# Optimization experiments

Measured on AMD Instinct MI355X. Metric: run time of the kernel, lower is better.

The kernel has to match this reference:

```python
import jax, jax.numpy as jnp
import numpy as np

B, T, D, H, L = 16, 1500, 512, 1024, 20


def setup_inputs() -> dict:
    key = jax.random.key(0)
    ks = jax.random.split(key, 5)
    return {
        "x": jax.random.normal(ks[0], (B, T, D), dtype=jnp.float32),
        "w1": jax.random.normal(ks[1], (D, H), dtype=jnp.float32) * (1.0 / np.sqrt(D)),
        "b1": jax.random.normal(ks[2], (H,), dtype=jnp.float32) * 0.01,
        "wp": jax.random.normal(ks[3], (H, D), dtype=jnp.float32) * (1.0 / np.sqrt(H)),
        "wa": jax.random.normal(ks[4], (D, L), dtype=jnp.float32) * (1.0 / np.sqrt(D)),
    }


def reference(x, w1, b1, wp, wa):
    # x: [B,T,D]
    f1 = jax.nn.relu(x @ w1 + b1)          # [B,T,H]
    p1 = f1 @ wp                            # [B,T,D] (output_dim == input_dim)
    lorder = wa.shape[1]
    t = p1.shape[1]
    # left-pad time axis with lorder-1 zeros so shift i looks at p1[t-i]
    padded = jnp.pad(p1, ((0, 0), (lorder - 1, 0), (0, 0)))  # [B,T+L-1,D]
    # z[..., i] = p1 shifted back by i frames (zero for t-i < 0)
    z = jnp.stack(
        [jax.lax.dynamic_slice_in_dim(padded, lorder - 1 - i, t, axis=1)
         for i in range(lorder)],
        axis=-1,
    )  # [B,T,D,L]
    att = jax.nn.softmax(x @ wa, axis=-1)   # [B,T,L]
    out1 = jnp.einsum('btdl,btl->btd', z, att)
    return x + out1
```

## Files before the change

### kernel.cpp

```cpp
#include <hip/hip_runtime.h>
#include <hip/hip_bf16.h>

#define Bd 16
#define Td 1500
#define Dd 512
#define Hd 1024
#define Ld 20
#define Md (Bd*Td)

using f32x4  = __attribute__((ext_vector_type(4))) float;
using short8 = __attribute__((ext_vector_type(8))) short;

__device__ __forceinline__ unsigned short f2bf(float f) {
    union { float f; unsigned u; } v; v.f = f;
    unsigned r = v.u + 0x7fffu + ((v.u >> 16) & 1u);
    return (unsigned short)(r >> 16);
}
__device__ __forceinline__ float bf2f(unsigned short u) {
    union { unsigned u; float f; } v; v.u = ((unsigned)u) << 16;
    return v.f;
}
__device__ __forceinline__ void gload_lds16(const void* g, void* l) {
    __builtin_amdgcn_global_load_lds(
        (const __attribute__((address_space(1))) unsigned*)g,
        (__attribute__((address_space(3))) unsigned*)l, 16, 0, 0);
}

__global__ __launch_bounds__(256) void cvt_x_kernel(
    const float* __restrict__ in, unsigned short* __restrict__ out)
{
    size_t i = ((size_t)blockIdx.x * 256 + threadIdx.x) * 8;
    float4 v0 = *(const float4*)(in + i);
    float4 v1 = *(const float4*)(in + i + 4);
    union { unsigned short us[8]; int4 v; } p;
    p.us[0] = f2bf(v0.x); p.us[1] = f2bf(v0.y); p.us[2] = f2bf(v0.z); p.us[3] = f2bf(v0.w);
    p.us[4] = f2bf(v1.x); p.us[5] = f2bf(v1.y); p.us[6] = f2bf(v1.z); p.us[7] = f2bf(v1.w);
    *(int4*)(out + i) = p.v;
}

__global__ __launch_bounds__(256) void transpose_convert_k(
    const float* __restrict__ W, unsigned short* __restrict__ WT, int K, int N)
{
    __shared__ float tile[32][33];
    int n0 = blockIdx.x * 32, k0 = blockIdx.y * 32;
    int tx = threadIdx.x, ty = threadIdx.y;
#pragma unroll
    for (int j = 0; j < 32; j += 8)
        tile[ty + j][tx] = W[(size_t)(k0 + ty + j) * N + n0 + tx];
    __syncthreads();
#pragma unroll
    for (int j = 0; j < 32; j += 8)
        WT[(size_t)(n0 + ty + j) * K + k0 + tx] = f2bf(tile[tx][ty + j]);
}

__global__ __launch_bounds__(256) void prep_waT_kernel(
    const float* __restrict__ wa, unsigned short* __restrict__ waT)
{
    int i = blockIdx.x * 256 + threadIdx.x;
    int c = i >> 9, d = i & 511;
    waT[i] = (c < Ld) ? f2bf(wa[(size_t)d * Ld + c]) : (unsigned short)0;
}

template<bool RELU_BIAS>
__global__ __launch_bounds__(256) void gemm_lds(
    const unsigned short* __restrict__ A, const unsigned short* __restrict__ BT,
    const float* __restrict__ bias, unsigned short* __restrict__ C,
    int Mdim, int Ndim, int Kdim)
{
    __shared__ __align__(16) unsigned short SH[2][3][128 * 32];

    const int tid  = threadIdx.x;
    const int lane = tid & 63;
    const int wave = tid >> 6;
    const int wr   = wave >> 1, wc = wave & 1;

    const int nx  = gridDim.x;
    const int nwg = nx * gridDim.y;
    const int id  = blockIdx.y * nx + blockIdx.x;
    const int nid = (id & 7) * (nwg >> 3) + (id >> 3);
    const int m0  = (nid / nx) * 128;
    const int n0  = (nid % nx) * 128;

    const int srow  = tid >> 2;
    const int sslot = (tid & 3) ^ ((tid >> 3) & 3);
    int ar0 = m0 + srow;      if (ar0 >= Mdim) ar0 = Mdim - 1;
    int ar1 = m0 + 64 + srow; if (ar1 >= Mdim) ar1 = Mdim - 1;
    const unsigned short* a0p = A  + (size_t)ar0 * Kdim + sslot * 8;
    const unsigned short* a1p = A  + (size_t)ar1 * Kdim + sslot * 8;
    const unsigned short* b0p = BT + (size_t)(n0 + srow) * Kdim + sslot * 8;
    const unsigned short* b1p = BT + (size_t)(n0 + 64 + srow) * Kdim + sslot * 8;

    const int rsel = lane & 15;
    const int koff = ((lane >> 4) ^ ((lane >> 1) & 3)) * 8;

    f32x4 acc[4][4] = {};
    const int NT = Kdim >> 5;

    auto stage = [&](int t, int b) {
        const int kk = t * 32;
        gload_lds16(a0p + kk, &SH[0][b][wave * 512]);
        gload_lds16(a1p + kk, &SH[0][b][2048 + wave * 512]);
        gload_lds16(b0p + kk, &SH[1][b][wave * 512]);
        gload_lds16(b1p + kk, &SH[1][b][2048 + wave * 512]);
    };

    stage(0, 0);
    stage(1, 1);

    int buf = 0;
    for (int t = 0; t < NT; ++t) {
        if (t + 1 < NT) asm volatile("s_waitcnt vmcnt(4)" ::: "memory");
        else            asm volatile("s_waitcnt vmcnt(0)" ::: "memory");
        __builtin_amdgcn_s_barrier();
        asm volatile("" ::: "memory");

        if (t + 2 < NT) {
            int nb = buf + 2;
            if (nb >= 3) nb -= 3;
            stage(t + 2, nb);
        }

        const unsigned short* as = &SH[0][buf][0];
        const unsigned short* bs = &SH[1][buf][0];
        short8 af[4], bfr[4];
#pragma unroll
        for (int m = 0; m < 4; ++m)
            af[m] = *(const short8*)&as[(wr * 64 + m * 16 + rsel) * 32 + koff];
#pragma unroll
        for (int n = 0; n < 4; ++n)
            bfr[n] = *(const short8*)&bs[(wc * 64 + n * 16 + rsel) * 32 + koff];

        __builtin_amdgcn_s_setprio(1);
#pragma unroll
        for (int m = 0; m < 4; ++m)
#pragma unroll
            for (int n = 0; n < 4; ++n)
                acc[m][n] = __builtin_amdgcn_mfma_f32_16x16x32_bf16(af[m], bfr[n], acc[m][n], 0, 0, 0);
        __builtin_amdgcn_s_setprio(0);

        ++buf; if (buf == 3) buf = 0;
    }

    __syncthreads();
    unsigned short* Cs = (unsigned short*)SH;

    const int rB = wr * 64 + ((lane >> 4) << 2);
    const int cB = wc * 64;
#pragma unroll
    for (int n = 0; n < 4; ++n) {
        const int col = cB + n * 16 + rsel;
        float bvs = 0.f;
        if (RELU_BIAS) bvs = bias[n0 + col];
        const int s = col >> 3, e = col & 7;
#pragma unroll
        for (int m = 0; m < 4; ++m) {
#pragma unroll
            for (int j = 0; j < 4; ++j) {
                const int r = rB + m * 16 + j;
                float v = acc[m][n][j];
                if (RELU_BIAS) v = fmaxf(v + bvs, 0.f);
                Cs[r * 128 + ((s ^ (r & 7)) << 3) + e] = f2bf(v);
            }
        }
    }
    __syncthreads();

    const int row = tid >> 1;
    const int c0  = (tid & 1) * 64;
    const int gr  = m0 + row;
    if (gr < Mdim) {
#pragma unroll
        for (int i = 0; i < 8; ++i) {
            const int s = (c0 >> 3) + i;
            int4 v = *(const int4*)&Cs[row * 128 + ((s ^ (row & 7)) << 3)];
            *(int4*)&C[(size_t)gr * Ndim + n0 + c0 + i * 8] = v;
        }
    }
}

__global__ __launch_bounds__(256) void att_mfma_kernel(
    const unsigned short* __restrict__ xb, const unsigned short* __restrict__ waT,
    float* __restrict__ att)
{
    __shared__ __align__(16) unsigned short waTs[16 * 1024];
    __shared__ __align__(16) unsigned short As[3][64 * 32];
    __shared__ float sS[64][21];

    const int tid  = threadIdx.x;
    const int lane = tid & 63;
    const int wave = tid >> 6;
    const int m0   = blockIdx.x * 64;

    for (int i = tid; i < 2048; i += 256) {
        const int off = i * 8;
        const int kt = off >> 10, c = (off >> 5) & 31, sl = (off >> 3) & 3;
        const int ssl = sl ^ ((c >> 1) & 3);
        *(short8*)&waTs[off] = *(const short8*)&waT[(size_t)c * Dd + kt * 32 + ssl * 8];
    }
    __syncthreads();

    const int srow  = tid >> 2;
    const int sslot = (tid & 3) ^ ((tid >> 3) & 3);
    const unsigned short* a0p = xb + (size_t)(m0 + srow) * Dd + sslot * 8;

    const int rsel = lane & 15;
    const int koff = ((lane >> 4) ^ ((lane >> 1) & 3)) * 8;

    f32x4 acc[2] = {};

    gload_lds16(a0p, &As[0][wave * 512]);
    gload_lds16(a0p + 32, &As[1][wave * 512]);

    int buf = 0;
    for (int t = 0; t < 16; ++t) {
        if (t < 15) asm volatile("s_waitcnt vmcnt(1)" ::: "memory");
        else        asm volatile("s_waitcnt vmcnt(0)" ::: "memory");
        __builtin_amdgcn_s_barrier();
        asm volatile("" ::: "memory");

        if (t + 2 < 16) {
            int nb = buf + 2; if (nb >= 3) nb -= 3;
            gload_lds16(a0p + (t + 2) * 32, &As[nb][wave * 512]);
        }

        short8 af = *(const short8*)&As[buf][(wave * 16 + rsel) * 32 + koff];
        short8 b0 = *(const short8*)&waTs[t * 1024 + (rsel) * 32 + koff];
        short8 b1 = *(const short8*)&waTs[t * 1024 + (16 + rsel) * 32 + koff];
        acc[0] = __builtin_amdgcn_mfma_f32_16x16x32_bf16(af, b0, acc[0], 0, 0, 0);
        acc[1] = __builtin_amdgcn_mfma_f32_16x16x32_bf16(af, b1, acc[1], 0, 0, 0);

        ++buf; if (buf == 3) buf = 0;
    }

    const int r0 = wave * 16 + ((lane >> 4) << 2);
#pragma unroll
    for (int n = 0; n < 2; ++n) {
        const int c = n * 16 + rsel;
        if (c < 21) {
#pragma unroll
            for (int j = 0; j < 4; ++j)
                sS[r0 + j][c] = acc[n][j];
        }
    }
    __syncthreads();

    if (tid < 64) {
        float mx = -1e30f;
#pragma unroll
        for (int l = 0; l < Ld; ++l) mx = fmaxf(mx, sS[tid][l]);
        float e[Ld]; float sum = 0.f;
#pragma unroll
        for (int l = 0; l < Ld; ++l) { e[l] = __expf(sS[tid][l] - mx); sum += e[l]; }
        const float inv = 1.f / sum;
        const int grow = m0 + tid;
#pragma unroll
        for (int l = 0; l < Ld; ++l)
            att[(size_t)grow * Ld + l] = e[l] * inv;
    }
}

__global__ __launch_bounds__(512) void out_kernel(
    const float* __restrict__ x, const unsigned short* __restrict__ p1,
    const float* __restrict__ att, float* __restrict__ out)
{
    const int bid = blockIdx.x;
    const int nid = (bid & 7) * 375 + (bid >> 3);
    const int wave = threadIdx.x >> 6;
    const int lane = threadIdx.x & 63;
    const int row  = nid * 8 + wave;
    const int t    = row % Td;
    const int d0   = lane * 8;

    float av[Ld];
    const float* ar = att + (size_t)row * Ld;
#pragma unroll
    for (int i = 0; i < Ld; i += 4) {
        float4 v = *(const float4*)(ar + i);
        av[i] = v.x; av[i + 1] = v.y; av[i + 2] = v.z; av[i + 3] = v.w;
    }

    const float* xr = x + (size_t)row * Dd + d0;
    float4 xa = *(const float4*)xr;
    float4 xb4 = *(const float4*)(xr + 4);
    float acc[8] = { xa.x, xa.y, xa.z, xa.w, xb4.x, xb4.y, xb4.z, xb4.w };

    const int imax = (t < Ld - 1) ? t : (Ld - 1);
    const unsigned short* pr = p1 + (size_t)row * Dd + d0;
    for (int i = 0; i <= imax; ++i) {
        const float a = av[i];
        short8 p = *(const short8*)(pr - (size_t)i * Dd);
#pragma unroll
        for (int j = 0; j < 8; ++j) acc[j] += a * bf2f((unsigned short)p[j]);
    }
    float* orow = out + (size_t)row * Dd + d0;
    float4 o0 = { acc[0], acc[1], acc[2], acc[3] };
    float4 o1 = { acc[4], acc[5], acc[6], acc[7] };
    *(float4*)orow       = o0;
    *(float4*)(orow + 4) = o1;
}

extern "C" void kernel_launch(void* const* d_in, const int* in_sizes, int n_in,
                              void* d_out, int out_size, void* d_ws, size_t ws_size,
                              hipStream_t stream)
{
    const float* x  = (const float*)d_in[0];
    const float* w1 = (const float*)d_in[1];
    const float* b1 = (const float*)d_in[2];
    const float* wp = (const float*)d_in[3];
    const float* wa = (const float*)d_in[4];
    float* out = (float*)d_out;

    char* ws = (char*)d_ws;
    unsigned short* xb  = (unsigned short*)ws;  ws += (size_t)Md * Dd * 2;
    unsigned short* w1T = (unsigned short*)ws;  ws += (size_t)Hd * Dd * 2;
    unsigned short* wpT = (unsigned short*)ws;  ws += (size_t)Dd * Hd * 2;
    unsigned short* waT = (unsigned short*)ws;  ws += (size_t)32 * Dd * 2;
    unsigned short* f1  = (unsigned short*)ws;  ws += (size_t)Md * Hd * 2;
    unsigned short* p1  = (unsigned short*)ws;  ws += (size_t)Md * Dd * 2;
    float*          att = (float*)ws;           ws += (size_t)Md * Ld * 4;

    cvt_x_kernel<<<(Md * Dd) / 2048, 256, 0, stream>>>(x, xb);
    transpose_convert_k<<<dim3(Hd / 32, Dd / 32), dim3(32, 8), 0, stream>>>(w1, w1T, Dd, Hd);
    transpose_convert_k<<<dim3(Dd / 32, Hd / 32), dim3(32, 8), 0, stream>>>(wp, wpT, Hd, Dd);
    prep_waT_kernel<<<(32 * Dd) / 256, 256, 0, stream>>>(wa, waT);

    att_mfma_kernel<<<Md / 64, 256, 0, stream>>>(xb, waT, att);

    const int mtiles = (Md + 127) / 128;
    gemm_lds<true ><<<dim3(Hd / 128, mtiles), 256, 0, stream>>>(xb, w1T, b1, f1, Md, Hd, Dd);
    gemm_lds<false><<<dim3(Dd / 128, mtiles), 256, 0, stream>>>(f1, wpT, nullptr, p1, Md, Dd, Hd);

    out_kernel<<<Md / 8, 512, 0, stream>>>(x, p1, att, out);
}
```

Before: 226.5 us.

## Enlarge GEMM tiles to 256x128 with 512 threads and fuse prep kernels

The GEMM kernel moves from a 128x128 tile with 256 threads to a 256x128 tile with 512 threads (8 waves), so each B tile loaded into LDS is shared by twice as many rows. The goal is less global traffic per FLOP. The input conversion, the two weight transposes and the waT prep are merged into one launch, removing three kernel launches. In exchange the GEMM uses more LDS per block, has fewer blocks in flight, and has a larger partial tail tile at the M edge. The epilogue and wave-index code not shown must already handle 8 waves.

```diff
diff --git a/kernel.cpp b/kernel.cpp
--- a/kernel.cpp
+++ b/kernel.cpp
@@ -26,24 +26,11 @@
         (__attribute__((address_space(3))) unsigned*)l, 16, 0, 0);
 }
 
-__global__ __launch_bounds__(256) void cvt_x_kernel(
-    const float* __restrict__ in, unsigned short* __restrict__ out)
-{
-    size_t i = ((size_t)blockIdx.x * 256 + threadIdx.x) * 8;
-    float4 v0 = *(const float4*)(in + i);
-    float4 v1 = *(const float4*)(in + i + 4);
-    union { unsigned short us[8]; int4 v; } p;
-    p.us[0] = f2bf(v0.x); p.us[1] = f2bf(v0.y); p.us[2] = f2bf(v0.z); p.us[3] = f2bf(v0.w);
-    p.us[4] = f2bf(v1.x); p.us[5] = f2bf(v1.y); p.us[6] = f2bf(v1.z); p.us[7] = f2bf(v1.w);
-    *(int4*)(out + i) = p.v;
-}
-
-__global__ __launch_bounds__(256) void transpose_convert_k(
-    const float* __restrict__ W, unsigned short* __restrict__ WT, int K, int N)
-{
-    __shared__ float tile[32][33];
-    int n0 = blockIdx.x * 32, k0 = blockIdx.y * 32;
-    int tx = threadIdx.x, ty = threadIdx.y;
+__device__ __forceinline__ void transpose_body(
+    const float* __restrict__ W, unsigned short* __restrict__ WT,
+    int K, int N, int n0, int k0, int tid, float (*tile)[33])
+{
+    const int tx = tid & 31, ty = tid >> 5;
 #pragma unroll
     for (int j = 0; j < 32; j += 8)
         tile[ty + j][tx] = W[(size_t)(k0 + ty + j) * N + n0 + tx];
@@ -53,21 +40,42 @@
         WT[(size_t)(n0 + ty + j) * K + k0 + tx] = f2bf(tile[tx][ty + j]);
 }
 
-__global__ __launch_bounds__(256) void prep_waT_kernel(
-    const float* __restrict__ wa, unsigned short* __restrict__ waT)
-{
-    int i = blockIdx.x * 256 + threadIdx.x;
-    int c = i >> 9, d = i & 511;
-    waT[i] = (c < Ld) ? f2bf(wa[(size_t)d * Ld + c]) : (unsigned short)0;
+__global__ __launch_bounds__(256) void prep_kernel(
+    const float* __restrict__ x,  const float* __restrict__ w1,
+    const float* __restrict__ wp, const float* __restrict__ wa,
+    unsigned short* __restrict__ xb,  unsigned short* __restrict__ w1T,
+    unsigned short* __restrict__ wpT, unsigned short* __restrict__ waT)
+{
+    __shared__ float tile[32][33];
+    const int b = blockIdx.x, tid = threadIdx.x;
+    if (b < 6000) {
+        size_t i = ((size_t)b * 256 + tid) * 8;
+        float4 v0 = *(const float4*)(x + i);
+        float4 v1 = *(const float4*)(x + i + 4);
+        union { unsigned short us[8]; int4 v; } p;
+        p.us[0] = f2bf(v0.x); p.us[1] = f2bf(v0.y); p.us[2] = f2bf(v0.z); p.us[3] = f2bf(v0.w);
+        p.us[4] = f2bf(v1.x); p.us[5] = f2bf(v1.y); p.us[6] = f2bf(v1.z); p.us[7] = f2bf(v1.w);
+        *(int4*)(xb + i) = p.v;
+    } else if (b < 6512) {
+        const int idx = b - 6000;
+        transpose_body(w1, w1T, Dd, Hd, (idx & 31) * 32, (idx >> 5) * 32, tid, tile);
+    } else if (b < 7024) {
+        const int idx = b - 6512;
+        transpose_body(wp, wpT, Hd, Dd, (idx & 15) * 32, (idx >> 4) * 32, tid, tile);
+    } else {
+        const int i = (b - 7024) * 256 + tid;
+        const int c = i >> 9, d = i & 511;
+        waT[i] = (c < Ld) ? f2bf(wa[(size_t)d * Ld + c]) : (unsigned short)0;
+    }
 }
 
 template<bool RELU_BIAS>
-__global__ __launch_bounds__(256) void gemm_lds(
+__global__ __launch_bounds__(512) void gemm_lds(
     const unsigned short* __restrict__ A, const unsigned short* __restrict__ BT,
     const float* __restrict__ bias, unsigned short* __restrict__ C,
     int Mdim, int Ndim, int Kdim)
 {
-    __shared__ __align__(16) unsigned short SH[2][3][128 * 32];
+    __shared__ __align__(16) unsigned short SH[3 * 8192 + 3 * 4096];
 
     const int tid  = threadIdx.x;
     const int lane = tid & 63;
@@ -78,17 +86,16 @@
     const int nwg = nx * gridDim.y;
     const int id  = blockIdx.y * nx + blockIdx.x;
     const int nid = (id & 7) * (nwg >> 3) + (id >> 3);
-    const int m0  = (nid / nx) * 128;
+    const int m0  = (nid / nx) * 256;
     const int n0  = (nid % nx) * 128;
 
     const int srow  = tid >> 2;
-    const int sslot = (tid & 3) ^ ((tid >> 3) & 3);
-    int ar0 = m0 + srow;      if (ar0 >= Mdim) ar0 = Mdim - 1;
-    int ar1 = m0 + 64 + srow; if (ar1 >= Mdim) ar1 = Mdim - 1;
-    const unsigned short* a0p = A  + (size_t)ar0 * Kdim + sslot * 8;
-    const unsigned short* a1p = A  + (size_t)ar1 * Kdim + sslot * 8;
+    const int sslot = (tid & 3) ^ ((srow >> 1) & 3);
+    int aR0 = m0 + srow;       if (aR0 >= Mdim) aR0 = Mdim - 1;
+    int aR1 = m0 + 128 + srow; if (aR1 >= Mdim) aR1 = Mdim - 1;
+    const unsigned short* a0p = A  + (size_t)aR0 * Kdim + sslot * 8;
+    const unsigned short* a1p = A  + (size_t)aR1 * Kdim + sslot * 8;
     const unsigned short* b0p = BT + (size_t)(n0 + srow) * Kdim + sslot * 8;
-    const unsigned short* b1p = BT + (size_t)(n0 + 64 + srow) * Kdim + sslot * 8;
 
     const int rsel = lane & 15;
     const int koff = ((lane >> 4) ^ ((lane >> 1) & 3)) * 8;
@@ -98,10 +105,9 @@
 
     auto stage = [&](int t, int b) {
         const int kk = t * 32;
-        gload_lds16(a0p + kk, &SH[0][b][wave * 512]);
-        gload_lds16(a1p + kk, &SH[0][b][2048 + wave * 512]);
-        gload_lds16(b0p + kk, &SH[1][b][wave * 512]);
-        gload_lds16(b1p + kk, &SH[1][b][2048 + wave * 512]);
+        gload_lds16(a0p + kk, SH + b * 8192 + wave * 512);
+        gload_lds16(a1p + kk, SH + b * 8192 + 4096 + wave * 512);
+        gload_lds16(b0p + kk, SH + 24576 + b * 4096 + wave * 512);
     };
 
     stage(0, 0);
@@ -109,19 +115,18 @@
 
     int buf = 0;
     for (int t = 0; t < NT; ++t) {
-        if (t + 1 < NT) asm volatile("s_waitcnt vmcnt(4)" ::: "memory");
+        if (t + 1 < NT) asm volatile("s_waitcnt vmcnt(3)" ::: "memory");
         else            asm volatile("s_waitcnt vmcnt(0)" ::: "memory");
         __builtin_amdgcn_s_barrier();
         asm volatile("" ::: "memory");
 
         if (t + 2 < NT) {
-            int nb = buf + 2;
-            if (nb >= 3) nb -= 3;
+            int nb = buf + 2; if (nb >= 3) nb -= 3;
             stage(t + 2, nb);
         }
 
-        const unsigned short* as = &SH[0][buf][0];
-        const unsigned short* bs = &SH[1][buf][0];
+        const unsigned short* as = SH + buf * 8192;
+        const unsigned short* bs = SH + 24576 + buf * 4096;
         short8 af[4], bfr[4];
 #pragma unroll
         for (int m = 0; m < 4; ++m)
@@ -142,7 +147,7 @@
     }
 
     __syncthreads();
-    unsigned short* Cs = (unsigned short*)SH;
+    unsigned short* Cs = SH;
 
     const int rB = wr * 64 + ((lane >> 4) << 2);
     const int cB = wc * 64;
@@ -319,16 +324,13 @@
     unsigned short* p1  = (unsigned short*)ws;  ws += (size_t)Md * Dd * 2;
     float*          att = (float*)ws;           ws += (size_t)Md * Ld * 4;
 
-    cvt_x_kernel<<<(Md * Dd) / 2048, 256, 0, stream>>>(x, xb);
-    transpose_convert_k<<<dim3(Hd / 32, Dd / 32), dim3(32, 8), 0, stream>>>(w1, w1T, Dd, Hd);
-    transpose_convert_k<<<dim3(Dd / 32, Hd / 32), dim3(32, 8), 0, stream>>>(wp, wpT, Hd, Dd);
-    prep_waT_kernel<<<(32 * Dd) / 256, 256, 0, stream>>>(wa, waT);
+    prep_kernel<<<7088, 256, 0, stream>>>(x, w1, wp, wa, xb, w1T, wpT, waT);
 
     att_mfma_kernel<<<Md / 64, 256, 0, stream>>>(xb, waT, att);
 
-    const int mtiles = (Md + 127) / 128;
-    gemm_lds<true ><<<dim3(Hd / 128, mtiles), 256, 0, stream>>>(xb, w1T, b1, f1, Md, Hd, Dd);
-    gemm_lds<false><<<dim3(Dd / 128, mtiles), 256, 0, stream>>>(f1, wpT, nullptr, p1, Md, Dd, Hd);
+    const int mtiles = (Md + 255) / 256;
+    gemm_lds<true ><<<dim3(Hd / 128, mtiles), 512, 0, stream>>>(xb, w1T, b1, f1, Md, Hd, Dd);
+    gemm_lds<false><<<dim3(Dd / 128, mtiles), 512, 0, stream>>>(f1, wpT, nullptr, p1, Md, Dd, Hd);
 
     out_kernel<<<Md / 8, 512, 0, stream>>>(x, p1, att, out);
 }
```

Result: faster. 216.3 us (-4.5%).
